# Kernel optimization log

Hardware: AMD Instinct MI355X
Metric: run time of the kernel (lower is better)

Reference implementation:

```python
import jax, jax.numpy as jnp
import numpy as np

N, E, G, H, R, L = 10000, 320000, 16, 128, 32, 3
NUM_TYPES = 60
CUTOFF = 5.0


def setup_inputs() -> dict:
    key = jax.random.key(0)
    ks = jax.random.split(key, 32)
    s = 1.0 / np.sqrt(H)

    def w(k, shape, scale):
        return jax.random.normal(k, shape, jnp.float32) * scale

    return {
        'z': jax.random.randint(ks[0], (N,), 0, NUM_TYPES),
        'pos': jax.random.normal(ks[1], (N, 3), jnp.float32) * 3.0,
        'edge_index': jax.random.randint(ks[2], (2, E), 0, N),
        'batch': jnp.sort(jax.random.randint(ks[3], (N,), 0, G)),
        # learned params (per-layer params stacked on leading L axis)
        'emb': w(ks[4], (NUM_TYPES, H), 0.1),
        'atomic_ref': jnp.zeros((NUM_TYPES, 1), jnp.float32),
        'W_msg': w(ks[5], (L, H, H), s), 'b_msg': jnp.zeros((L, H), jnp.float32),
        'W_rbf': w(ks[6], (L, R, H), 1.0 / np.sqrt(R)),
        'Wg1': w(ks[7], (L, 2 * H + R, H), 1.0 / np.sqrt(2 * H + R)),
        'bg1': jnp.zeros((L, H), jnp.float32),
        'Wgv': w(ks[8], (L, H, H), s),
        'Wg2': w(ks[9], (L, H, H), s), 'bg2': jnp.zeros((L, H), jnp.float32),
        'Wd1': w(ks[10], (L, H, H), s), 'bd1': jnp.zeros((L, H), jnp.float32),
        'Wd2': w(ks[11], (L, H, H), s), 'bd2': jnp.zeros((L, H), jnp.float32),
        'Wr1': w(ks[12], (L, H, H), s), 'br1': jnp.zeros((L, H), jnp.float32),
        'Wr2': w(ks[13], (L, H, 1), s), 'br2': jnp.zeros((L, 1), jnp.float32),
        'num_graphs': G,
    }


def _rbf(d):
    # Gaussian radial basis with cosine cutoff envelope.  d: [E]
    centers = jnp.linspace(0.0, CUTOFF, R, dtype=d.dtype)
    gamma = (R / CUTOFF) ** 2
    fcut = 0.5 * (jnp.cos(jnp.pi * d / CUTOFF) + 1.0) * (d < CUTOFF)
    return jnp.exp(-gamma * (d[:, None] - centers) ** 2) * fcut[:, None]  # [E,R]


def reference(z, pos, edge_index, batch, emb, atomic_ref, W_msg, b_msg, W_rbf,
              Wg1, bg1, Wgv, Wg2, bg2, Wd1, bd1, Wd2, bd2, Wr1, br1, Wr2, br2,
              num_graphs):
    row, col = edge_index[0], edge_index[1]
    vec = pos[col] - pos[row]                       # [E,3] edge vectors
    d = jnp.clip(jnp.linalg.norm(vec, axis=-1), 1e-8, None)
    r_hat = vec / d[:, None]                        # [E,3]
    rbf = _rbf(d)                                   # [E,R]

    h0 = emb[z]                                     # [N,H] scalar features
    h1 = jnp.zeros((z.shape[0], 3, H), h0.dtype)    # [N,3,H] l=1 features
    e_tot = jnp.zeros((num_graphs, 1), h0.dtype)

    n_nodes = z.shape[0]
    for l in range(L):
        # LeibnizCoupling: radial-filtered edge messages
        m = (h0[col] @ W_msg[l] + b_msg[l]) * (rbf @ W_rbf[l])      # [E,H]
        # PhysicsGating: gate from endpoint scalars, rbf, and projected l=1 feats
        s1 = jnp.einsum('ech,ec->eh', h1[row], r_hat)               # [E,H]
        g_in = jnp.concatenate([h0[row], h0[col], rbf], axis=-1)
        pre = jax.nn.silu(g_in @ Wg1[l] + bg1[l] + s1 @ Wgv[l])
        gate = jax.nn.sigmoid(pre @ Wg2[l] + bg2[l])                # [E,H]
        gm = gate * m
        # CartesianDensityBlock: scatter messages to nodes
        agg = jax.ops.segment_sum(gm, row, num_segments=n_nodes)    # [N,H]
        delta_h0 = jax.nn.silu(agg @ Wd1[l] + bd1[l]) @ Wd2[l] + bd2[l]
        delta_h1 = jax.ops.segment_sum(r_hat[:, :, None] * gm[:, None, :],
                                       row, num_segments=n_nodes)   # [N,3,H]
        h0 = h0 + delta_h0
        h1 = h1 + delta_h1
        # per-layer readout -> per-graph energy
        e_atom = jax.nn.silu(h0 @ Wr1[l] + br1[l]) @ Wr2[l] + br2[l]  # [N,1]
        e_tot = e_tot + jax.ops.segment_sum(e_atom, batch, num_segments=num_graphs)

    e_tot = e_tot + jax.ops.segment_sum(atomic_ref[z], batch, num_segments=num_graphs)
    return e_tot
```

## Files before the change

kernel.cpp:

```cpp
#include <hip/hip_runtime.h>

#define HDIM 128
#define RDIM 32
#define BE   64
#define SB   2048

typedef __attribute__((ext_vector_type(8))) short s8v;
typedef __attribute__((ext_vector_type(4))) float f4v;

__device__ __forceinline__ float sigm(float x){ return 1.0f/(1.0f+__expf(-x)); }
__device__ __forceinline__ float silu_f(float x){ return x*sigm(x); }
__device__ __forceinline__ float4 f4z(){ return make_float4(0.f,0.f,0.f,0.f); }

__device__ __forceinline__ unsigned short f2bf(float x){
  unsigned u = __float_as_uint(x);
  unsigned r = u + 0x7FFFu + ((u>>16)&1u);
  return (unsigned short)(r>>16);
}
__device__ __forceinline__ float bf2f(unsigned short b){
  return __uint_as_float(((unsigned)b)<<16);
}

#define FMA4C(D, sc, W) do{ (D).x=fmaf((sc),(W).x,(D).x); (D).y=fmaf((sc),(W).y,(D).y); \
                            (D).z=fmaf((sc),(W).z,(D).z); (D).w=fmaf((sc),(W).w,(D).w);}while(0)
#define LERP4ADD(D, A0, A1, f) do{ \
  (D).x += fmaf((f),(A1).x-(A0).x,(A0).x); (D).y += fmaf((f),(A1).y-(A0).y,(A0).y); \
  (D).z += fmaf((f),(A1).z-(A0).z,(A0).z); (D).w += fmaf((f),(A1).w-(A0).w,(A0).w);}while(0)

__global__ __launch_bounds__(256) void k_init(const int* __restrict__ z,
                                              const float* __restrict__ emb,
                                              const int* __restrict__ batch,
                                              const float* __restrict__ aref,
                                              float* __restrict__ eout,
                                              float* __restrict__ h0,
                                              float* __restrict__ h1, int N, int G){
  __shared__ float bins[256];
  const int b = blockIdx.x, t = threadIdx.x;
  const int idx = b*256 + t;
  if (idx < N*HDIM){ int n = idx>>7, h = idx&127; h0[idx] = emb[z[n]*HDIM + h]; }
  if (idx < N*384) h1[idx] = 0.f;
  if (b < (N+255)/256){
    for (int i=t;i<G;i+=256) bins[i]=0.f;
    __syncthreads();
    if (idx < N) atomicAdd(&bins[batch[idx]], aref[z[idx]]);
    __syncthreads();
    for (int i=t;i<G;i+=256) if (bins[i]!=0.f) unsafeAtomicAdd(&eout[i], bins[i]);
  }
}

__global__ __launch_bounds__(256) void k_geom(const float* __restrict__ pos,
                                              const int* __restrict__ eidx, int E,
                                              int* __restrict__ ecnt,
                                              int* __restrict__ erow, int* __restrict__ ecol,
                                              float* __restrict__ erx, float* __restrict__ ery,
                                              float* __restrict__ erz, float* __restrict__ ed,
                                              int* __restrict__ cnt){
  __shared__ int scan[256];
  __shared__ int sbase;
  int t = threadIdx.x;
  int e = blockIdx.x*256 + t;
  int alive = 0; float dx=0,dy=0,dz=0,d=1.f; int row=0,col=0;
  if (e < E){
    row = eidx[e]; col = eidx[E+e];
    float ax=pos[row*3+0], ay=pos[row*3+1], az=pos[row*3+2];
    float bx=pos[col*3+0], by=pos[col*3+1], bz=pos[col*3+2];
    dx=bx-ax; dy=by-ay; dz=bz-az;
    d = sqrtf(dx*dx+dy*dy+dz*dz);
    d = fmaxf(d, 1e-8f);
    alive = (d < 5.0f) ? 1 : 0;
  }
  scan[t]=alive; __syncthreads();
  for (int off=1; off<256; off<<=1){
    int v = (t>=off)? scan[t-off] : 0;
    __syncthreads();
    if (t>=off) scan[t]+=v;
    __syncthreads();
  }
  if (t==255) sbase = atomicAdd(ecnt, scan[255]);
  __syncthreads();
  if (alive){
    int p = sbase + scan[t]-1;
    erow[p]=row; ecol[p]=col;
    float inv = 1.0f/d;
    erx[p]=dx*inv; ery[p]=dy*inv; erz[p]=dz*inv;
    ed[p]=d;
    atomicAdd(&cnt[row], 1);
  }
}

__global__ __launch_bounds__(1024) void k_scan(const int* __restrict__ cnt,
                                               int* __restrict__ estart, int N){
  __shared__ int ps[1024];
  const int t = threadIdx.x;
  const int CH = (N + 1023)/1024;
  const int base = t*CH;
  int s = 0;
  for (int i=0;i<CH;i++){ int idx=base+i; if(idx<N) s += cnt[idx]; }
  ps[t] = s; __syncthreads();
  for (int off=1; off<1024; off<<=1){
    int v = (t>=off)? ps[t-off]:0;
    __syncthreads();
    ps[t]+=v;
    __syncthreads();
  }
  int run = (t==0)? 0 : ps[t-1];
  for (int i=0;i<CH;i++){
    int idx=base+i;
    if (idx<N){ estart[idx]=run; run += cnt[idx]; }
  }
  if (t==1023) estart[N] = ps[1023];
}

__global__ __launch_bounds__(256) void k_fill(const int* __restrict__ ecnt,
                                              const int* __restrict__ erow,
                                              const int* __restrict__ ecol,
                                              const float* __restrict__ erx,
                                              const float* __restrict__ ery,
                                              const float* __restrict__ erz,
                                              const float* __restrict__ ed,
                                              const int* __restrict__ estart,
                                              int* __restrict__ fillc, int CAP,
                                              int* __restrict__ srow, int* __restrict__ scol,
                                              float* __restrict__ srx, float* __restrict__ sry,
                                              float* __restrict__ srz, float* __restrict__ sd){
  int e = blockIdx.x*256 + threadIdx.x;
  if (e < ecnt[0]){
    int r = erow[e];
    int pos = estart[r] + atomicAdd(&fillc[r], 1);
    if (pos < CAP){
      srow[pos]=r; scol[pos]=ecol[e];
      srx[pos]=erx[e]; sry[pos]=ery[e]; srz[pos]=erz[e]; sd[pos]=ed[e];
    }
  }
}

__global__ __launch_bounds__(128) void k_lutcvt(const float* __restrict__ Wg1,
                                                const float* __restrict__ Wrbf,
                                                float* __restrict__ Tg, float* __restrict__ Tr,
                                                const float* __restrict__ Wmsg,
                                                const float* __restrict__ Wgv,
                                                const float* __restrict__ Wd1,
                                                const float* __restrict__ Wd2,
                                                const float* __restrict__ Wr1,
                                                const float* __restrict__ Wg2,
                                                unsigned short* __restrict__ WT, int L){
  const int b = blockIdx.x;
  if (b < L*SB){
    const int l = b / SB;
    const int s = b % SB;
    __shared__ float rbf[RDIM];
    const float d = s * (5.0f/(SB-1));
    if (threadIdx.x < RDIM){
      float fc = 0.5f*(__cosf(0.62831853071f*d)+1.0f);
      float td = d - 0.16129032258f*threadIdx.x;
      rbf[threadIdx.x] = __expf(-40.96f*td*td)*fc;
    }
    __syncthreads();
    const int c = threadIdx.x;
    const float* Wg = Wg1 + (size_t)l*288*HDIM + 256*HDIM;
    const float* Wr = Wrbf + (size_t)l*RDIM*HDIM;
    float sg=0.f, sr=0.f;
    #pragma unroll
    for (int r=0;r<RDIM;r++){
      sg = fmaf(rbf[r], Wg[r*HDIM+c], sg);
      sr = fmaf(rbf[r], Wr[r*HDIM+c], sr);
    }
    Tg[((size_t)l*SB+s)*HDIM + c] = sg;
    Tr[((size_t)l*SB+s)*HDIM + c] = sr;
    return;
  }
  const int base = (b - L*SB)*1024;
  #pragma unroll
  for (int u=0;u<8;u++){
    int idx = base + u*128 + threadIdx.x;
    if (idx >= L*8*16384) return;
    int l = idx / (8*16384);
    int rem = idx % (8*16384);
    int mat = rem >> 14;
    int nk = rem & 16383;
    int n = nk >> 7, k = nk & 127;
    float v;
    switch(mat){
      case 0: v = Wmsg[(size_t)l*16384 + k*128 + n]; break;
      case 1: v = Wg1 [(size_t)l*288*128 + k*128 + n]; break;
      case 2: v = Wg1 [(size_t)l*288*128 + (128+k)*128 + n]; break;
      case 3: v = Wgv [(size_t)l*16384 + k*128 + n]; break;
      case 4: v = Wd1 [(size_t)l*16384 + k*128 + n]; break;
      case 5: v = Wd2 [(size_t)l*16384 + k*128 + n]; break;
      case 6: v = Wr1 [(size_t)l*16384 + k*128 + n]; break;
      default: v = Wg2[(size_t)l*16384 + k*128 + n]; break;
    }
    WT[idx] = f2bf(v);
  }
}

__device__ __forceinline__ void stage32p(float (*WS)[132], const float* __restrict__ W, int t){
  int r = t>>3, c0 = (t&7)*16;
  const float4* src = (const float4*)&W[(size_t)r*HDIM + c0];
  float4* dst = (float4*)&WS[r][c0];
  #pragma unroll
  for (int u=0;u<4;u++) dst[u]=src[u];
}

__device__ __forceinline__ void load_tile(float (*S)[132], const float* __restrict__ src,
                                          int nb, int N, int stride, int t){
  #pragma unroll
  for (int u=0;u<4;u++){
    int p = t + 256*u;
    int r = p>>5, c4 = p&31;
    float4 v = f4z();
    if (nb + r < N) v = *(const float4*)&src[(size_t)(nb+r)*stride + c4*4];
    *(float4*)&S[r][c4*4] = v;
  }
}

__device__ __forceinline__ void load_tile16(unsigned short (*S)[136], const float* __restrict__ src,
                                            int nb, int N, int stride, int t){
  #pragma unroll
  for (int u=0;u<4;u++){
    int p = t + 256*u;
    int r = p>>5, c4 = p&31;
    float4 v = f4z();
    if (nb + r < N) v = *(const float4*)&src[(size_t)(nb+r)*stride + c4*4];
    ushort4 pk; pk.x=f2bf(v.x); pk.y=f2bf(v.y); pk.z=f2bf(v.z); pk.w=f2bf(v.w);
    *(ushort4*)&S[r][c4*4] = pk;
  }
}

__device__ __forceinline__ void gemm_lds(const float (*AS)[132], float (*WS)[132],
                                         const float* __restrict__ W, const float* __restrict__ bias,
                                         int r, int cg, int t, float4 (&acc)[4]){
  float4 b = bias ? *(const float4*)&bias[4*cg] : f4z();
  #pragma unroll
  for (int i=0;i<4;i++) acc[i] = b;
  for (int kt=0; kt<4; kt++){
    stage32p(WS, W + (size_t)kt*32*HDIM, t);
    __syncthreads();
    #pragma unroll
    for (int k4=0;k4<8;k4++){
      float4 w0 = *(const float4*)&WS[4*k4+0][4*cg];
      float4 w1 = *(const float4*)&WS[4*k4+1][4*cg];
      float4 w2 = *(const float4*)&WS[4*k4+2][4*cg];
      float4 w3 = *(const float4*)&WS[4*k4+3][4*cg];
      #pragma unroll
      for (int i=0;i<4;i++){
        float4 a4 = *(const float4*)&AS[r+8*i][kt*32+4*k4];
        FMA4C(acc[i], a4.x, w0); FMA4C(acc[i], a4.y, w1);
        FMA4C(acc[i], a4.z, w2); FMA4C(acc[i], a4.w, w3);
      }
    }
    __syncthreads();
  }
}

__device__ __forceinline__ void mfma32(const unsigned short (*A16)[136],
                                       unsigned short (*WTs)[40],
                                       const unsigned short* __restrict__ WT,
                                       int t, f4v (&acc)[2][2]){
  const int lane = t&63, w = t>>6;
  const int l15 = lane&15, lk = lane>>4;
  for (int kt=0; kt<4; kt++){
    int n = t>>1, ch = t&1;
    *(s8v*)&WTs[n][ch*16]     = *(const s8v*)&WT[(size_t)n*HDIM + kt*32 + ch*16];
    *(s8v*)&WTs[n][ch*16 + 8] = *(const s8v*)&WT[(size_t)n*HDIM + kt*32 + ch*16 + 8];
    __syncthreads();
    s8v a0 = *(const s8v*)&A16[l15][kt*32 + lk*8];
    s8v a1 = *(const s8v*)&A16[16+l15][kt*32 + lk*8];
    s8v b0 = *(const s8v*)&WTs[w*32 +  0 + l15][lk*8];
    s8v b1 = *(const s8v*)&WTs[w*32 + 16 + l15][lk*8];
    acc[0][0] = __builtin_amdgcn_mfma_f32_16x16x32_bf16(a0, b0, acc[0][0], 0, 0, 0);
    acc[0][1] = __builtin_amdgcn_mfma_f32_16x16x32_bf16(a0, b1, acc[0][1], 0, 0, 0);
    acc[1][0] = __builtin_amdgcn_mfma_f32_16x16x32_bf16(a1, b0, acc[1][0], 0, 0, 0);
    acc[1][1] = __builtin_amdgcn_mfma_f32_16x16x32_bf16(a1, b1, acc[1][1], 0, 0, 0);
    __syncthreads();
  }
}

__device__ __forceinline__ void mfma16(const unsigned short (*A16)[136],
                                       unsigned short (*WTs)[40],
                                       const unsigned short* __restrict__ WT,
                                       int t, f4v (&acc)[2]){
  const int lane = t&63, w = t>>6;
  const int l15 = lane&15, lk = lane>>4;
  for (int kt=0; kt<4; kt++){
    int n = t>>1, ch = t&1;
    *(s8v*)&WTs[n][ch*16]     = *(const s8v*)&WT[(size_t)n*HDIM + kt*32 + ch*16];
    *(s8v*)&WTs[n][ch*16 + 8] = *(const s8v*)&WT[(size_t)n*HDIM + kt*32 + ch*16 + 8];
    __syncthreads();
    s8v a0 = *(const s8v*)&A16[l15][kt*32 + lk*8];
    s8v b0 = *(const s8v*)&WTs[w*32 +  0 + l15][lk*8];
    s8v b1 = *(const s8v*)&WTs[w*32 + 16 + l15][lk*8];
    acc[0] = __builtin_amdgcn_mfma_f32_16x16x32_bf16(a0, b0, acc[0], 0, 0, 0);
    acc[1] = __builtin_amdgcn_mfma_f32_16x16x32_bf16(a0, b1, acc[1], 0, 0, 0);
    __syncthreads();
  }
}

__global__ __launch_bounds__(256) void k_node_pre(const float* __restrict__ h0,
                                                  const float* __restrict__ h1,
                                                  const unsigned short* __restrict__ WTl,
                                                  const float* __restrict__ bmsg,
                                                  const float* __restrict__ bg1,
                                                  const float* __restrict__ Wr1p, const float* __restrict__ br1p,
                                                  const float* __restrict__ Wr2p, const float* __restrict__ br2p,
                                                  const int* __restrict__ batch, float* __restrict__ eout,
                                                  int G, int doRead,
                                                  float* __restrict__ hm, float* __restrict__ ga,
                                                  float* __restrict__ gb, float* __restrict__ hv, int N){
  __shared__ char smem[34816];
  const int t = threadIdx.x;
  const int g = blockIdx.y;
  const int nb = blockIdx.x*32;

  if (g == 6){
    if (!doRead) return;
    float (*AS)[132] = (float(*)[132])smem;
    float (*WS)[132] = (float(*)[132])(smem + 16896);
    float* ebins     = (float*)(smem + 33792);
    const int r = t>>5, cg = t&31;
    float4 acc[4];
    for (int i=t;i<G;i+=256) ebins[i]=0.f;
    load_tile(AS, h0, nb, N, HDIM, t);
    __syncthreads();
    gemm_lds(AS, WS, Wr1p, br1p, r, cg, t, acc);
    const float4 w2 = *(const float4*)&Wr2p[4*cg];
    float part[4];
    #pragma unroll
    for (int i=0;i<4;i++){
      float4 u;
      u.x=silu_f(acc[i].x); u.y=silu_f(acc[i].y);
      u.z=silu_f(acc[i].z); u.w=silu_f(acc[i].w);
      part[i] = u.x*w2.x + u.y*w2.y + u.z*w2.z + u.w*w2.w;
    }
    #pragma unroll
    for (int off=16; off>=1; off>>=1){
      #pragma unroll
      for (int i=0;i<4;i++) part[i] += __shfl_down(part[i], off, 32);
    }
    if (cg == 0){
      #pragma unroll
      for (int i=0;i<4;i++){
        int n = nb + r + 8*i;
        if (n < N) atomicAdd(&ebins[batch[n]], part[i] + br2p[0]);
      }
    }
    __syncthreads();
    for (int i=t;i<G;i+=256) if (ebins[i]!=0.f) unsafeAtomicAdd(&eout[i], ebins[i]);
    return;
  }

  unsigned short (*AS16)[136] = (unsigned short(*)[136])smem;
  unsigned short (*WTs)[40]   = (unsigned short(*)[40])(smem + 8704);

  const float* A; int astride;
  const float* bias;
  float* out; int ostride; int ooff; int mat;
  if (g < 3){
    A = h0; astride = HDIM;
    if (g==0){ mat = 0; bias = bmsg; out = hm; }
    else if (g==1){ mat = 1; bias = bg1;  out = ga; }
    else { mat = 2; bias = nullptr; out = gb; }
    ostride = HDIM; ooff = 0;
  } else {
    int c = g-3;
    A = h1 + c*HDIM; astride = 384;
    mat = 3; bias = nullptr;
    out = hv; ostride = 384; ooff = c*HDIM;
  }

  load_tile16(AS16, A, nb, N, astride, t);
  __syncthreads();

  f4v zz = {0.f,0.f,0.f,0.f};
  f4v acc[2][2]; acc[0][0]=zz; acc[0][1]=zz; acc[1][0]=zz; acc[1][1]=zz;
  mfma32(AS16, WTs, WTl + (size_t)mat*16384, t, acc);

  const int lane = t&63, w = t>>6, l15 = lane&15, lk = lane>>4;
  #pragma unroll
  for (int m=0;m<2;m++){
    #pragma unroll
    for (int ct=0;ct<2;ct++){
      int c = w*32 + ct*16 + l15;
      float bv = bias ? bias[c] : 0.f;
      #pragma unroll
      for (int reg=0;reg<4;reg++){
        int n = nb + m*16 + lk*4 + reg;
        if (n < N) out[(size_t)n*ostride + ooff + c] = acc[m][ct][reg] + bv;
      }
    }
  }
}

__global__ __launch_bounds__(256) void k_readout(const float* __restrict__ h0,
                                                 const float* __restrict__ Wr1, const float* __restrict__ br1,
                                                 const float* __restrict__ Wr2, const float* __restrict__ br2,
                                                 const int* __restrict__ batch, float* __restrict__ eout,
                                                 int N, int G){
  __shared__ float AS[32][132];
  __shared__ float WS[32][132];
  __shared__ float ebins[256];
  const int t = threadIdx.x;
  const int nb = blockIdx.x*32;
  const int r = t>>5, cg = t&31;
  float4 acc[4];
  for (int i=t;i<G;i+=256) ebins[i]=0.f;
  load_tile(AS, h0, nb, N, HDIM, t);
  __syncthreads();
  gemm_lds(AS, WS, Wr1, br1, r, cg, t, acc);
  const float4 w2 = *(const float4*)&Wr2[4*cg];
  float part[4];
  #pragma unroll
  for (int i=0;i<4;i++){
    float4 u;
    u.x=silu_f(acc[i].x); u.y=silu_f(acc[i].y);
    u.z=silu_f(acc[i].z); u.w=silu_f(acc[i].w);
    part[i] = u.x*w2.x + u.y*w2.y + u.z*w2.z + u.w*w2.w;
  }
  #pragma unroll
  for (int off=16; off>=1; off>>=1){
    #pragma unroll
    for (int i=0;i<4;i++) part[i] += __shfl_down(part[i], off, 32);
  }
  if (cg == 0){
    #pragma unroll
    for (int i=0;i<4;i++){
      int n = nb + r + 8*i;
      if (n < N) atomicAdd(&ebins[batch[n]], part[i] + br2[0]);
    }
  }
  __syncthreads();
  for (int i=t;i<G;i+=256) if (ebins[i]!=0.f) unsafeAtomicAdd(&eout[i], ebins[i]);
}

__global__ __launch_bounds__(512) void k_edge_gm(const int* __restrict__ ecnt, int CAP,
                                                 const int* __restrict__ srow, const int* __restrict__ scol,
                                                 const float* __restrict__ srx, const float* __restrict__ sry,
                                                 const float* __restrict__ srz, const float* __restrict__ sd,
                                                 const float* __restrict__ hm, const float* __restrict__ ga,
                                                 const float* __restrict__ gb, const float* __restrict__ hv,
                                                 const float* __restrict__ Tg,  const float* __restrict__ Tr,
                                                 const unsigned short* __restrict__ Wg2T,
                                                 const float* __restrict__ bg2,
                                                 unsigned short* __restrict__ gm_s){
  __shared__ unsigned short preA[BE][136];
  __shared__ unsigned short WTs[128][40];
  __shared__ int   rowS[BE], colS[BE];
  __shared__ float rhS[3][BE];
  __shared__ float fS[BE];
  __shared__ int   iS[BE];

  const int t = threadIdx.x;
  int ec = ecnt[0]; if (ec > CAP) ec = CAP;
  const int base = blockIdx.x*BE;
  if (base >= ec) return;

  if (t < BE){
    int eg = base + t;
    bool ok = eg < ec;
    rowS[t] = ok ? srow[eg] : 0;
    colS[t] = ok ? scol[eg] : 0;
    rhS[0][t] = ok ? srx[eg] : 0.f;
    rhS[1][t] = ok ? sry[eg] : 0.f;
    rhS[2][t] = ok ? srz[eg] : 0.f;
    float d = ok ? sd[eg] : 0.f;
    float u = d * ((float)(SB-1)/5.0f);
    int i = (int)u; if (i > SB-2) i = SB-2;
    iS[t] = i; fS[t] = u - (float)i;
  }
  __syncthreads();

  {
    const int e = t>>3, q = t&7;
    const int eg = base + e;
    const bool ok = eg < ec;
    const int row = rowS[e], col = colS[e];
    const float rx = rhS[0][e], ry = rhS[1][e], rz = rhS[2][e];
    const float ff = fS[e];
    const float4* tg0 = (const float4*)(Tg + (size_t)iS[e]*HDIM);
    const float4* tg1 = tg0 + (HDIM/4);
    const float4* gaR = (const float4*)(ga + (size_t)row*HDIM);
    const float4* gbR = (const float4*)(gb + (size_t)col*HDIM);
    const float4* hv0 = (const float4*)(hv + (size_t)row*384);
    const float4* hv1 = hv0 + 32;
    const float4* hv2 = hv0 + 64;
    #pragma unroll
    for (int j=0;j<4;j++){
      int cb = q + 8*j;
      float4 v = f4z();
      if (ok){
        float4 A = gaR[cb], B = gbR[cb];
        float4 V0 = hv0[cb], V1 = hv1[cb], V2 = hv2[cb];
        v.x = A.x+B.x; v.y = A.y+B.y; v.z = A.z+B.z; v.w = A.w+B.w;
        FMA4C(v, rx, V0); FMA4C(v, ry, V1); FMA4C(v, rz, V2);
        float4 a0 = tg0[cb], a1 = tg1[cb];
        LERP4ADD(v, a0, a1, ff);
        v.x = silu_f(v.x); v.y = silu_f(v.y); v.z = silu_f(v.z); v.w = silu_f(v.w);
      }
      ushort4 pk;
      pk.x = f2bf(v.x); pk.y = f2bf(v.y); pk.z = f2bf(v.z); pk.w = f2bf(v.w);
      *(ushort4*)&preA[e][4*cb] = pk;
    }
  }
  __syncthreads();

  const int lane = t & 63;
  const int w    = t >> 6;
  const int wm   = w & 3;
  const int wn   = w >> 2;
  const int l15  = lane & 15;
  const int lk   = lane >> 4;
  f4v acc0 = {0.f,0.f,0.f,0.f}, acc1 = acc0, acc2 = acc0, acc3 = acc0;

  for (int kt=0; kt<4; kt++){
    {
      int n = t>>2, ch = t&3;
      *(s8v*)&WTs[n][ch*8] = *(const s8v*)&Wg2T[(size_t)n*HDIM + kt*32 + ch*8];
    }
    __syncthreads();
    s8v a = *(const s8v*)&preA[wm*16 + l15][kt*32 + lk*8];
    s8v b0 = *(const s8v*)&WTs[wn*64 +  0 + l15][lk*8];
    s8v b1 = *(const s8v*)&WTs[wn*64 + 16 + l15][lk*8];
    s8v b2 = *(const s8v*)&WTs[wn*64 + 32 + l15][lk*8];
    s8v b3 = *(const s8v*)&WTs[wn*64 + 48 + l15][lk*8];
    acc0 = __builtin_amdgcn_mfma_f32_16x16x32_bf16(a, b0, acc0, 0, 0, 0);
    acc1 = __builtin_amdgcn_mfma_f32_16x16x32_bf16(a, b1, acc1, 0, 0, 0);
    acc2 = __builtin_amdgcn_mfma_f32_16x16x32_bf16(a, b2, acc2, 0, 0, 0);
    acc3 = __builtin_amdgcn_mfma_f32_16x16x32_bf16(a, b3, acc3, 0, 0, 0);
    __syncthreads();
  }

  {
    #pragma unroll
    for (int reg=0; reg<4; reg++){
      int m = lk*4 + reg;
      int e = wm*16 + m;
      preA[e][wn*64 +  0 + l15] = f2bf(acc0[reg]);
      preA[e][wn*64 + 16 + l15] = f2bf(acc1[reg]);
      preA[e][wn*64 + 32 + l15] = f2bf(acc2[reg]);
      preA[e][wn*64 + 48 + l15] = f2bf(acc3[reg]);
    }
  }
  __syncthreads();

  const int cg = t&31;
  const int e0 = (t>>5)*4;
  const float4 bg = *(const float4*)&bg2[4*cg];
  #pragma unroll
  for (int i=0;i<4;i++){
    int e = e0 + i;
    int eg = base + e;
    if (eg >= ec) continue;
    int col = colS[e];
    const float ff = fS[e];
    const float4* tr0 = (const float4*)(Tr + (size_t)iS[e]*HDIM);
    const float4* tr1 = tr0 + (HDIM/4);
    float4 r0 = tr0[cg], r1 = tr1[cg];
    float4 rw;
    rw.x = fmaf(ff, r1.x-r0.x, r0.x); rw.y = fmaf(ff, r1.y-r0.y, r0.y);
    rw.z = fmaf(ff, r1.z-r0.z, r0.z); rw.w = fmaf(ff, r1.w-r0.w, r0.w);
    float4 hmv = *(const float4*)&hm[(size_t)col*HDIM + 4*cg];
    ushort4 gp4 = *(const ushort4*)&preA[e][4*cg];
    float4 g;
    g.x = sigm(bf2f(gp4.x) + bg.x); g.y = sigm(bf2f(gp4.y) + bg.y);
    g.z = sigm(bf2f(gp4.z) + bg.z); g.w = sigm(bf2f(gp4.w) + bg.w);
    ushort4 pk;
    pk.x = f2bf(g.x*hmv.x*rw.x); pk.y = f2bf(g.y*hmv.y*rw.y);
    pk.z = f2bf(g.z*hmv.z*rw.z); pk.w = f2bf(g.w*hmv.w*rw.w);
    *(ushort4*)&gm_s[(size_t)eg*HDIM + 4*cg] = pk;
  }
}

__global__ __launch_bounds__(256) void k_node_post(float* __restrict__ h0, float* __restrict__ h1,
                                                   const int* __restrict__ estart, int CAP,
                                                   const unsigned short* __restrict__ gm_s,
                                                   const float* __restrict__ srx,
                                                   const float* __restrict__ sry,
                                                   const float* __restrict__ srz,
                                                   const unsigned short* __restrict__ WTd1,
                                                   const float* __restrict__ bd1,
                                                   const unsigned short* __restrict__ WTd2,
                                                   const float* __restrict__ bd2,
                                                   int N){
  __shared__ char smem[23040];
  float (*aS)[132]            = (float(*)[132])smem;
  unsigned short (*AS16)[136] = (unsigned short(*)[136])(smem+8448);
  unsigned short (*WTs)[40]   = (unsigned short(*)[40])(smem+12800);
  unsigned short (*tS16)[136] = (unsigned short(*)[136])smem;
  const int t = threadIdx.x;
  const int nb = blockIdx.x*16;

  {
    const int nl = t>>4, s = t&15;
    const int n = nb + nl;
    float4 ag[2], v0[2], v1[2], v2[2];
    #pragma unroll
    for (int j=0;j<2;j++){ ag[j]=f4z(); v0[j]=f4z(); v1[j]=f4z(); v2[j]=f4z(); }
    if (n < N){
      int p0 = estart[n];
      int p1 = estart[n+1]; if (p1 > CAP) p1 = CAP;
      for (int p=p0; p<p1; ++p){
        float rx = srx[p], ry = sry[p], rz = srz[p];
        const ushort4* gp = (const ushort4*)&gm_s[(size_t)p*HDIM + 8*s];
        #pragma unroll
        for (int j=0;j<2;j++){
          ushort4 pk = gp[j];
          float4 g;
          g.x = bf2f(pk.x); g.y = bf2f(pk.y); g.z = bf2f(pk.z); g.w = bf2f(pk.w);
          ag[j].x+=g.x; ag[j].y+=g.y; ag[j].z+=g.z; ag[j].w+=g.w;
          FMA4C(v0[j], rx, g); FMA4C(v1[j], ry, g); FMA4C(v2[j], rz, g);
        }
      }
    }
    #pragma unroll
    for (int j=0;j<2;j++) *(float4*)&aS[nl][8*s+4*j] = ag[j];
    if (n < N){
      #pragma unroll
      for (int j=0;j<2;j++){
        size_t b = (size_t)n*384 + 8*s + 4*j;
        float4 a0 = *(const float4*)&h1[b];
        float4 a1 = *(const float4*)&h1[b+128];
        float4 a2 = *(const float4*)&h1[b+256];
        a0.x+=v0[j].x; a0.y+=v0[j].y; a0.z+=v0[j].z; a0.w+=v0[j].w;
        a1.x+=v1[j].x; a1.y+=v1[j].y; a1.z+=v1[j].z; a1.w+=v1[j].w;
        a2.x+=v2[j].x; a2.y+=v2[j].y; a2.z+=v2[j].z; a2.w+=v2[j].w;
        *(float4*)&h1[b]     = a0;
        *(float4*)&h1[b+128] = a1;
        *(float4*)&h1[b+256] = a2;
      }
    }
  }
  __syncthreads();

  {
    #pragma unroll
    for (int u=0;u<2;u++){
      int p = t + 256*u;
      int r = p>>5, c4 = p&31;
      float4 v = *(const float4*)&aS[r][c4*4];
      ushort4 pk; pk.x=f2bf(v.x); pk.y=f2bf(v.y); pk.z=f2bf(v.z); pk.w=f2bf(v.w);
      *(ushort4*)&AS16[r][c4*4] = pk;
    }
  }
  __syncthreads();

  const int lane = t&63, w = t>>6, l15 = lane&15, lk = lane>>4;
  f4v zz = {0.f,0.f,0.f,0.f};
  f4v acc[2]; acc[0]=zz; acc[1]=zz;

  mfma16((const unsigned short(*)[136])AS16, WTs, WTd1, t, acc);
  #pragma unroll
  for (int ct=0;ct<2;ct++){
    int c = w*32 + ct*16 + l15;
    float bv = bd1[c];
    #pragma unroll
    for (int reg=0;reg<4;reg++){
      int rr = lk*4 + reg;
      tS16[rr][c] = f2bf(silu_f(acc[ct][reg] + bv));
    }
  }
  __syncthreads();

  acc[0]=zz; acc[1]=zz;
  mfma16((const unsigned short(*)[136])tS16, WTs, WTd2, t, acc);
  #pragma unroll
  for (int ct=0;ct<2;ct++){
    int c = w*32 + ct*16 + l15;
    float bv = bd2[c];
    #pragma unroll
    for (int reg=0;reg<4;reg++){
      int n = nb + lk*4 + reg;
      if (n < N) h0[(size_t)n*HDIM + c] += acc[ct][reg] + bv;
    }
  }
}

extern "C" void kernel_launch(void* const* d_in, const int* in_sizes, int n_in,
                              void* d_out, int out_size, void* d_ws, size_t ws_size,
                              hipStream_t stream){
  const int*   z     = (const int*)  d_in[0];
  const float* pos   = (const float*)d_in[1];
  const int*   eidx  = (const int*)  d_in[2];
  const int*   batch = (const int*)  d_in[3];
  const float* emb   = (const float*)d_in[4];
  const float* aref  = (const float*)d_in[5];
  const float* Wmsg  = (const float*)d_in[6];
  const float* bmsg  = (const float*)d_in[7];
  const float* Wrbf  = (const float*)d_in[8];
  const float* Wg1   = (const float*)d_in[9];
  const float* bg1   = (const float*)d_in[10];
  const float* Wgv   = (const float*)d_in[11];
  const float* Wg2   = (const float*)d_in[12];
  const float* bg2   = (const float*)d_in[13];
  const float* Wd1   = (const float*)d_in[14];
  const float* bd1   = (const float*)d_in[15];
  const float* Wd2   = (const float*)d_in[16];
  const float* bd2   = (const float*)d_in[17];
  const float* Wr1   = (const float*)d_in[18];
  const float* br1   = (const float*)d_in[19];
  const float* Wr2   = (const float*)d_in[20];
  const float* br2   = (const float*)d_in[21];
  const int N = in_sizes[0];
  const int E = in_sizes[2]/2;
  const int G = out_size;
  const int L = 3;
  const int CAP = (int)(((long long)E*7)/16);
  float* out = (float*)d_out;

  char* ws = (char*)d_ws;
  size_t off = 0;
  auto carve = [&](size_t bytes)->char*{
    char* p = ws + off; off += (bytes + 255) & ~(size_t)255; return p;
  };
  char*  zero0  = ws;
  int*   ecnt   = (int*)  carve(sizeof(int));
  int*   cnt    = (int*)  carve((size_t)N*4);
  int*   fillc  = (int*)  carve((size_t)N*4);
  size_t zlen   = off;
  int*   erow   = (int*)  carve((size_t)E*4);
  int*   ecol   = (int*)  carve((size_t)E*4);
  float* erx    = (float*)carve((size_t)E*4);
  float* ery    = (float*)carve((size_t)E*4);
  float* erz    = (float*)carve((size_t)E*4);
  float* ed     = (float*)carve((size_t)E*4);
  int*   estart = (int*)  carve((size_t)(N+1)*4);
  int*   srow   = (int*)  carve((size_t)CAP*4);
  int*   scol   = (int*)  carve((size_t)CAP*4);
  float* srx    = (float*)carve((size_t)CAP*4);
  float* sry    = (float*)carve((size_t)CAP*4);
  float* srz    = (float*)carve((size_t)CAP*4);
  float* sd     = (float*)carve((size_t)CAP*4);
  unsigned short* gm_s = (unsigned short*)carve((size_t)CAP*HDIM*2);
  unsigned short* WT   = (unsigned short*)carve((size_t)L*8*HDIM*HDIM*2);
  float* Tg     = (float*)carve((size_t)L*SB*HDIM*4);
  float* Tr     = (float*)carve((size_t)L*SB*HDIM*4);
  float* h0     = (float*)carve((size_t)N*HDIM*4);
  float* h1b    = (float*)carve((size_t)N*384*4);
  float* hm     = (float*)carve((size_t)N*HDIM*4);
  float* ga     = (float*)carve((size_t)N*HDIM*4);
  float* gb     = (float*)carve((size_t)N*HDIM*4);
  float* hvb    = (float*)carve((size_t)N*384*4);

  (void)hipMemsetAsync(zero0, 0, zlen, stream);
  (void)hipMemsetAsync(out,   0, (size_t)G*4, stream);

  k_init<<<(N*384+255)/256, 256, 0, stream>>>(z, emb, batch, aref, out, h0, h1b, N, G);
  k_geom<<<(E+255)/256, 256, 0, stream>>>(pos, eidx, E, ecnt, erow, ecol, erx, ery, erz, ed, cnt);
  {
    int cvt_blocks = (L*8*16384 + 1023)/1024;
    k_lutcvt<<<L*SB + cvt_blocks, 128, 0, stream>>>(Wg1, Wrbf, Tg, Tr,
                                                    Wmsg, Wgv, Wd1, Wd2, Wr1, Wg2, WT, L);
  }
  k_scan<<<1, 1024, 0, stream>>>(cnt, estart, N);
  k_fill<<<(E+255)/256, 256, 0, stream>>>(ecnt, erow, ecol, erx, ery, erz, ed,
                                          estart, fillc, CAP,
                                          srow, scol, srx, sry, srz, sd);

  const int nblk   = (N+31)/32;
  const int nblk16 = (N+15)/16;
  const int eblk   = (CAP + BE-1)/BE;
  for (int l=0; l<L; ++l){
    const int lp = (l>0) ? (l-1) : 0;
    const unsigned short* WTl = WT + (size_t)l*8*16384;
    k_node_pre<<<dim3(nblk,7), 256, 0, stream>>>(h0, h1b,
        WTl,
        bmsg + (size_t)l*HDIM, bg1 + (size_t)l*HDIM,
        Wr1 + (size_t)lp*HDIM*HDIM, br1 + (size_t)lp*HDIM,
        Wr2 + (size_t)lp*HDIM, br2 + lp,
        batch, out, G, (l>0) ? 1 : 0,
        hm, ga, gb, hvb, N);
    k_edge_gm<<<eblk, 512, 0, stream>>>(ecnt, CAP, srow, scol, srx, sry, srz, sd,
        hm, ga, gb, hvb,
        Tg + (size_t)l*SB*HDIM, Tr + (size_t)l*SB*HDIM,
        WTl + (size_t)7*16384, bg2 + (size_t)l*HDIM,
        gm_s);
    k_node_post<<<nblk16, 256, 0, stream>>>(h0, h1b, estart, CAP, gm_s, srx, sry, srz,
        WTl + (size_t)4*16384, bd1 + (size_t)l*HDIM,
        WTl + (size_t)5*16384, bd2 + (size_t)l*HDIM,
        N);
  }
  k_readout<<<nblk, 256, 0, stream>>>(h0,
      Wr1 + (size_t)(L-1)*HDIM*HDIM, br1 + (size_t)(L-1)*HDIM,
      Wr2 + (size_t)(L-1)*HDIM, br2 + (L-1),
      batch, out, N, G);
}
```

Before: 328.4 us.

## Fuse node-post, next-layer node-pre projections and readout into one kernel

Merges the per-layer node update (aggregation plus Wd1/Wd2 MLP), the next layer's node projections (Wmsg, Wg1 halves, Wgv on h1) and the energy readout into a single kernel working on 16-node tiles. The updated h0 and h1 stay in LDS as bf16, so they are not re-read from global memory, and two launches per layer are removed. The readout GEMM moves from an fp32 FMA path to bf16 MFMA, which costs some precision. Each fused block now runs many sequential small GEMMs, which may lower parallelism compared with the separate 2D-grid node_pre launch.

```diff
diff --git a/kernel.cpp b/kernel.cpp
--- a/kernel.cpp
+++ b/kernel.cpp
@@ -194,26 +194,6 @@
   }
 }
 
-__device__ __forceinline__ void stage32p(float (*WS)[132], const float* __restrict__ W, int t){
-  int r = t>>3, c0 = (t&7)*16;
-  const float4* src = (const float4*)&W[(size_t)r*HDIM + c0];
-  float4* dst = (float4*)&WS[r][c0];
-  #pragma unroll
-  for (int u=0;u<4;u++) dst[u]=src[u];
-}
-
-__device__ __forceinline__ void load_tile(float (*S)[132], const float* __restrict__ src,
-                                          int nb, int N, int stride, int t){
-  #pragma unroll
-  for (int u=0;u<4;u++){
-    int p = t + 256*u;
-    int r = p>>5, c4 = p&31;
-    float4 v = f4z();
-    if (nb + r < N) v = *(const float4*)&src[(size_t)(nb+r)*stride + c4*4];
-    *(float4*)&S[r][c4*4] = v;
-  }
-}
-
 __device__ __forceinline__ void load_tile16(unsigned short (*S)[136], const float* __restrict__ src,
                                             int nb, int N, int stride, int t){
   #pragma unroll
@@ -227,32 +207,6 @@
   }
 }
 
-__device__ __forceinline__ void gemm_lds(const float (*AS)[132], float (*WS)[132],
-                                         const float* __restrict__ W, const float* __restrict__ bias,
-                                         int r, int cg, int t, float4 (&acc)[4]){
-  float4 b = bias ? *(const float4*)&bias[4*cg] : f4z();
-  #pragma unroll
-  for (int i=0;i<4;i++) acc[i] = b;
-  for (int kt=0; kt<4; kt++){
-    stage32p(WS, W + (size_t)kt*32*HDIM, t);
-    __syncthreads();
-    #pragma unroll
-    for (int k4=0;k4<8;k4++){
-      float4 w0 = *(const float4*)&WS[4*k4+0][4*cg];
-      float4 w1 = *(const float4*)&WS[4*k4+1][4*cg];
-      float4 w2 = *(const float4*)&WS[4*k4+2][4*cg];
-      float4 w3 = *(const float4*)&WS[4*k4+3][4*cg];
-      #pragma unroll
-      for (int i=0;i<4;i++){
-        float4 a4 = *(const float4*)&AS[r+8*i][kt*32+4*k4];
-        FMA4C(acc[i], a4.x, w0); FMA4C(acc[i], a4.y, w1);
-        FMA4C(acc[i], a4.z, w2); FMA4C(acc[i], a4.w, w3);
-      }
-    }
-    __syncthreads();
-  }
-}
-
 __device__ __forceinline__ void mfma32(const unsigned short (*A16)[136],
                                        unsigned short (*WTs)[40],
                                        const unsigned short* __restrict__ WT,
@@ -301,56 +255,13 @@
                                                   const unsigned short* __restrict__ WTl,
                                                   const float* __restrict__ bmsg,
                                                   const float* __restrict__ bg1,
-                                                  const float* __restrict__ Wr1p, const float* __restrict__ br1p,
-                                                  const float* __restrict__ Wr2p, const float* __restrict__ br2p,
-                                                  const int* __restrict__ batch, float* __restrict__ eout,
-                                                  int G, int doRead,
                                                   float* __restrict__ hm, float* __restrict__ ga,
                                                   float* __restrict__ gb, float* __restrict__ hv, int N){
-  __shared__ char smem[34816];
+  __shared__ unsigned short AS16[32][136];
+  __shared__ unsigned short WTs[128][40];
   const int t = threadIdx.x;
   const int g = blockIdx.y;
   const int nb = blockIdx.x*32;
-
-  if (g == 6){
-    if (!doRead) return;
-    float (*AS)[132] = (float(*)[132])smem;
-    float (*WS)[132] = (float(*)[132])(smem + 16896);
-    float* ebins     = (float*)(smem + 33792);
-    const int r = t>>5, cg = t&31;
-    float4 acc[4];
-    for (int i=t;i<G;i+=256) ebins[i]=0.f;
-    load_tile(AS, h0, nb, N, HDIM, t);
-    __syncthreads();
-    gemm_lds(AS, WS, Wr1p, br1p, r, cg, t, acc);
-    const float4 w2 = *(const float4*)&Wr2p[4*cg];
-    float part[4];
-    #pragma unroll
-    for (int i=0;i<4;i++){
-      float4 u;
-      u.x=silu_f(acc[i].x); u.y=silu_f(acc[i].y);
-      u.z=silu_f(acc[i].z); u.w=silu_f(acc[i].w);
-      part[i] = u.x*w2.x + u.y*w2.y + u.z*w2.z + u.w*w2.w;
-    }
-    #pragma unroll
-    for (int off=16; off>=1; off>>=1){
-      #pragma unroll
-      for (int i=0;i<4;i++) part[i] += __shfl_down(part[i], off, 32);
-    }
-    if (cg == 0){
-      #pragma unroll
-      for (int i=0;i<4;i++){
-        int n = nb + r + 8*i;
-        if (n < N) atomicAdd(&ebins[batch[n]], part[i] + br2p[0]);
-      }
-    }
-    __syncthreads();
-    for (int i=t;i<G;i+=256) if (ebins[i]!=0.f) unsafeAtomicAdd(&eout[i], ebins[i]);
-    return;
-  }
-
-  unsigned short (*AS16)[136] = (unsigned short(*)[136])smem;
-  unsigned short (*WTs)[40]   = (unsigned short(*)[40])(smem + 8704);
 
   const float* A; int astride;
   const float* bias;
@@ -373,7 +284,7 @@
 
   f4v zz = {0.f,0.f,0.f,0.f};
   f4v acc[2][2]; acc[0][0]=zz; acc[0][1]=zz; acc[1][0]=zz; acc[1][1]=zz;
-  mfma32(AS16, WTs, WTl + (size_t)mat*16384, t, acc);
+  mfma32((const unsigned short(*)[136])AS16, WTs, WTl + (size_t)mat*16384, t, acc);
 
   const int lane = t&63, w = t>>6, l15 = lane&15, lk = lane>>4;
   #pragma unroll
@@ -389,47 +300,6 @@
       }
     }
   }
-}
-
-__global__ __launch_bounds__(256) void k_readout(const float* __restrict__ h0,
-                                                 const float* __restrict__ Wr1, const float* __restrict__ br1,
-                                                 const float* __restrict__ Wr2, const float* __restrict__ br2,
-                                                 const int* __restrict__ batch, float* __restrict__ eout,
-                                                 int N, int G){
-  __shared__ float AS[32][132];
-  __shared__ float WS[32][132];
-  __shared__ float ebins[256];
-  const int t = threadIdx.x;
-  const int nb = blockIdx.x*32;
-  const int r = t>>5, cg = t&31;
-  float4 acc[4];
-  for (int i=t;i<G;i+=256) ebins[i]=0.f;
-  load_tile(AS, h0, nb, N, HDIM, t);
-  __syncthreads();
-  gemm_lds(AS, WS, Wr1, br1, r, cg, t, acc);
-  const float4 w2 = *(const float4*)&Wr2[4*cg];
-  float part[4];
-  #pragma unroll
-  for (int i=0;i<4;i++){
-    float4 u;
-    u.x=silu_f(acc[i].x); u.y=silu_f(acc[i].y);
-    u.z=silu_f(acc[i].z); u.w=silu_f(acc[i].w);
-    part[i] = u.x*w2.x + u.y*w2.y + u.z*w2.z + u.w*w2.w;
-  }
-  #pragma unroll
-  for (int off=16; off>=1; off>>=1){
-    #pragma unroll
-    for (int i=0;i<4;i++) part[i] += __shfl_down(part[i], off, 32);
-  }
-  if (cg == 0){
-    #pragma unroll
-    for (int i=0;i<4;i++){
-      int n = nb + r + 8*i;
-      if (n < N) atomicAdd(&ebins[batch[n]], part[i] + br2[0]);
-    }
-  }
-  __syncthreads();
-  for (int i=t;i<G;i+=256) if (ebins[i]!=0.f) unsafeAtomicAdd(&eout[i], ebins[i]);
 }
 
 __global__ __launch_bounds__(512) void k_edge_gm(const int* __restrict__ ecnt, int CAP,
@@ -570,24 +440,36 @@
   }
 }
 
-__global__ __launch_bounds__(256) void k_node_post(float* __restrict__ h0, float* __restrict__ h1,
-                                                   const int* __restrict__ estart, int CAP,
-                                                   const unsigned short* __restrict__ gm_s,
-                                                   const float* __restrict__ srx,
-                                                   const float* __restrict__ sry,
-                                                   const float* __restrict__ srz,
-                                                   const unsigned short* __restrict__ WTd1,
-                                                   const float* __restrict__ bd1,
-                                                   const unsigned short* __restrict__ WTd2,
-                                                   const float* __restrict__ bd2,
-                                                   int N){
-  __shared__ char smem[23040];
-  float (*aS)[132]            = (float(*)[132])smem;
-  unsigned short (*AS16)[136] = (unsigned short(*)[136])(smem+8448);
-  unsigned short (*WTs)[40]   = (unsigned short(*)[40])(smem+12800);
-  unsigned short (*tS16)[136] = (unsigned short(*)[136])smem;
+__global__ __launch_bounds__(256) void k_fused(float* __restrict__ h0, float* __restrict__ h1,
+                                               const int* __restrict__ estart, int CAP,
+                                               const unsigned short* __restrict__ gm_s,
+                                               const float* __restrict__ srx,
+                                               const float* __restrict__ sry,
+                                               const float* __restrict__ srz,
+                                               const unsigned short* __restrict__ WTcur,
+                                               const unsigned short* __restrict__ WTnxt,
+                                               const float* __restrict__ bd1,
+                                               const float* __restrict__ bd2,
+                                               const float* __restrict__ bmsgN,
+                                               const float* __restrict__ bg1N,
+                                               const float* __restrict__ br1,
+                                               const float* __restrict__ Wr2,
+                                               const float* __restrict__ br2p,
+                                               const int* __restrict__ batch,
+                                               float* __restrict__ eout, int G,
+                                               float* __restrict__ hm, float* __restrict__ ga,
+                                               float* __restrict__ gb, float* __restrict__ hv,
+                                               int doPre, int N){
+  __shared__ unsigned short AS16[16][136];
+  __shared__ unsigned short h0S[16][136];
+  __shared__ unsigned short h1S[3][16][136];
+  __shared__ unsigned short WTs[128][40];
+  __shared__ float ebins[256];
   const int t = threadIdx.x;
   const int nb = blockIdx.x*16;
+  const int lane = t&63, w = t>>6, l15 = lane&15, lk = lane>>4;
+
+  for (int i=t;i<256;i+=256) ebins[i]=0.f;
 
   {
     const int nl = t>>4, s = t&15;
@@ -612,7 +494,11 @@
       }
     }
     #pragma unroll
-    for (int j=0;j<2;j++) *(float4*)&aS[nl][8*s+4*j] = ag[j];
+    for (int j=0;j<2;j++){
+      ushort4 pk;
+      pk.x=f2bf(ag[j].x); pk.y=f2bf(ag[j].y); pk.z=f2bf(ag[j].z); pk.w=f2bf(ag[j].w);
+      *(ushort4*)&AS16[nl][8*s+4*j] = pk;
+    }
     if (n < N){
       #pragma unroll
       for (int j=0;j<2;j++){
@@ -626,42 +512,42 @@
         *(float4*)&h1[b]     = a0;
         *(float4*)&h1[b+128] = a1;
         *(float4*)&h1[b+256] = a2;
+        ushort4 p0s; p0s.x=f2bf(a0.x); p0s.y=f2bf(a0.y); p0s.z=f2bf(a0.z); p0s.w=f2bf(a0.w);
+        ushort4 p1s; p1s.x=f2bf(a1.x); p1s.y=f2bf(a1.y); p1s.z=f2bf(a1.z); p1s.w=f2bf(a1.w);
+        ushort4 p2s; p2s.x=f2bf(a2.x); p2s.y=f2bf(a2.y); p2s.z=f2bf(a2.z); p2s.w=f2bf(a2.w);
+        *(ushort4*)&h1S[0][nl][8*s+4*j] = p0s;
+        *(ushort4*)&h1S[1][nl][8*s+4*j] = p1s;
+        *(ushort4*)&h1S[2][nl][8*s+4*j] = p2s;
       }
-    }
-  }
-  __syncthreads();
-
-  {
-    #pragma unroll
-    for (int u=0;u<2;u++){
-      int p = t + 256*u;
-      int r = p>>5, c4 = p&31;
-      float4 v = *(const float4*)&aS[r][c4*4];
-      ushort4 pk; pk.x=f2bf(v.x); pk.y=f2bf(v.y); pk.z=f2bf(v.z); pk.w=f2bf(v.w);
-      *(ushort4*)&AS16[r][c4*4] = pk;
-    }
-  }
-  __syncthreads();
-
-  const int lane = t&63, w = t>>6, l15 = lane&15, lk = lane>>4;
+    } else {
+      ushort4 zq = {0,0,0,0};
+      #pragma unroll
+      for (int j=0;j<2;j++){
+        *(ushort4*)&h1S[0][nl][8*s+4*j] = zq;
+        *(ushort4*)&h1S[1][nl][8*s+4*j] = zq;
+        *(ushort4*)&h1S[2][nl][8*s+4*j] = zq;
+      }
+    }
+  }
+  __syncthreads();
+
   f4v zz = {0.f,0.f,0.f,0.f};
-  f4v acc[2]; acc[0]=zz; acc[1]=zz;
-
-  mfma16((const unsigned short(*)[136])AS16, WTs, WTd1, t, acc);
+  f4v acc[2];
+
+  acc[0]=zz; acc[1]=zz;
+  mfma16((const unsigned short(*)[136])AS16, WTs, WTcur + (size_t)4*16384, t, acc);
   #pragma unroll
   for (int ct=0;ct<2;ct++){
     int c = w*32 + ct*16 + l15;
     float bv = bd1[c];
     #pragma unroll
-    for (int reg=0;reg<4;reg++){
-      int rr = lk*4 + reg;
-      tS16[rr][c] = f2bf(silu_f(acc[ct][reg] + bv));
-    }
+    for (int reg=0;reg<4;reg++)
+      h0S[lk*4+reg][c] = f2bf(silu_f(acc[ct][reg] + bv));
   }
   __syncthreads();
 
   acc[0]=zz; acc[1]=zz;
-  mfma16((const unsigned short(*)[136])tS16, WTs, WTd2, t, acc);
+  mfma16((const unsigned short(*)[136])h0S, WTs, WTcur + (size_t)5*16384, t, acc);
   #pragma unroll
   for (int ct=0;ct<2;ct++){
     int c = w*32 + ct*16 + l15;
@@ -669,9 +555,76 @@
     #pragma unroll
     for (int reg=0;reg<4;reg++){
       int n = nb + lk*4 + reg;
-      if (n < N) h0[(size_t)n*HDIM + c] += acc[ct][reg] + bv;
-    }
-  }
+      float h = (n<N) ? h0[(size_t)n*HDIM + c] : 0.f;
+      h += acc[ct][reg] + bv;
+      if (n<N) h0[(size_t)n*HDIM + c] = h;
+      h0S[lk*4+reg][c] = f2bf(h);
+    }
+  }
+  __syncthreads();
+
+  if (doPre){
+    #pragma unroll
+    for (int mat=0; mat<3; mat++){
+      const float* bias = (mat==0)? bmsgN : (mat==1)? bg1N : nullptr;
+      float* out = (mat==0)? hm : (mat==1)? ga : gb;
+      acc[0]=zz; acc[1]=zz;
+      mfma16((const unsigned short(*)[136])h0S, WTs, WTnxt + (size_t)mat*16384, t, acc);
+      #pragma unroll
+      for (int ct=0;ct<2;ct++){
+        int c = w*32 + ct*16 + l15;
+        float bv = bias ? bias[c] : 0.f;
+        #pragma unroll
+        for (int reg=0;reg<4;reg++){
+          int n = nb + lk*4 + reg;
+          if (n<N) out[(size_t)n*HDIM + c] = acc[ct][reg] + bv;
+        }
+      }
+      __syncthreads();
+    }
+    #pragma unroll
+    for (int cdim=0; cdim<3; cdim++){
+      acc[0]=zz; acc[1]=zz;
+      mfma16((const unsigned short(*)[136])h1S[cdim], WTs, WTnxt + (size_t)3*16384, t, acc);
+      #pragma unroll
+      for (int ct=0;ct<2;ct++){
+        int c = w*32 + ct*16 + l15;
+        #pragma unroll
+        for (int reg=0;reg<4;reg++){
+          int n = nb + lk*4 + reg;
+          if (n<N) hv[(size_t)n*384 + cdim*HDIM + c] = acc[ct][reg];
+        }
+      }
+      __syncthreads();
+    }
+  }
+
+  acc[0]=zz; acc[1]=zz;
+  mfma16((const unsigned short(*)[136])h0S, WTs, WTcur + (size_t)6*16384, t, acc);
+  #pragma unroll
+  for (int ct=0;ct<2;ct++){
+    int c = w*32 + ct*16 + l15;
+    float bv = br1[c];
+    #pragma unroll
+    for (int reg=0;reg<4;reg++)
+      AS16[lk*4+reg][c] = f2bf(silu_f(acc[ct][reg] + bv));
+  }
+  __syncthreads();
+  {
+    const int nl = t>>4, s = t&15;
+    const int n = nb + nl;
+    float part = 0.f;
+    #pragma unroll
+    for (int i=0;i<8;i++){
+      int c = 8*s + i;
+      part = fmaf(bf2f(AS16[nl][c]), Wr2[c], part);
+    }
+    #pragma unroll
+    for (int off=8; off>=1; off>>=1) part += __shfl_down(part, off, 16);
+    if (s==0 && n<N) atomicAdd(&ebins[batch[n]], part + br2p[0]);
+  }
+  __syncthreads();
+  for (int i=t;i<G;i+=256) if (ebins[i]!=0.f) unsafeAtomicAdd(&eout[i], ebins[i]);
 }
 
 extern "C" void kernel_launch(void* const* d_in, const int* in_sizes, int n_in,
@@ -758,28 +711,26 @@
   const int nblk   = (N+31)/32;
   const int nblk16 = (N+15)/16;
   const int eblk   = (CAP + BE-1)/BE;
+
+  k_node_pre<<<dim3(nblk,6), 256, 0, stream>>>(h0, h1b,
+      WT, bmsg, bg1, hm, ga, gb, hvb, N);
+
   for (int l=0; l<L; ++l){
-    const int lp = (l>0) ? (l-1) : 0;
-    const unsigned short* WTl = WT + (size_t)l*8*16384;
-    k_node_pre<<<dim3(nblk,7), 256, 0, stream>>>(h0, h1b,
-        WTl,
-        bmsg + (size_t)l*HDIM, bg1 + (size_t)l*HDIM,
-        Wr1 + (size_t)lp*HDIM*HDIM, br1 + (size_t)lp*HDIM,
-        Wr2 + (size_t)lp*HDIM, br2 + lp,
-        batch, out, G, (l>0) ? 1 : 0,
-        hm, ga, gb, hvb, N);
+    const unsigned short* WTcur = WT + (size_t)l*8*16384;
+    const int ln = (l<L-1) ? (l+1) : l;
+    const unsigned short* WTnxt = WT + (size_t)ln*8*16384;
     k_edge_gm<<<eblk, 512, 0, stream>>>(ecnt, CAP, srow, scol, srx, sry, srz, sd,
         hm, ga, gb, hvb,
         Tg + (size_t)l*SB*HDIM, Tr + (size_t)l*SB*HDIM,
-        WTl + (size_t)7*16384, bg2 + (size_t)l*HDIM,
+        WTcur + (size_t)7*16384, bg2 + (size_t)l*HDIM,
         gm_s);
-    k_node_post<<<nblk16, 256, 0, stream>>>(h0, h1b, estart, CAP, gm_s, srx, sry, srz,
-        WTl + (size_t)4*16384, bd1 + (size_t)l*HDIM,
-        WTl + (size_t)5*16384, bd2 + (size_t)l*HDIM,
-        N);
-  }
-  k_readout<<<nblk, 256, 0, stream>>>(h0,
-      Wr1 + (size_t)(L-1)*HDIM*HDIM, br1 + (size_t)(L-1)*HDIM,
-      Wr2 + (size_t)(L-1)*HDIM, br2 + (L-1),
-      batch, out, N, G);
-}
+    k_fused<<<nblk16, 256, 0, stream>>>(h0, h1b, estart, CAP, gm_s, srx, sry, srz,
+        WTcur, WTnxt,
+        bd1 + (size_t)l*HDIM, bd2 + (size_t)l*HDIM,
+        bmsg + (size_t)ln*HDIM, bg1 + (size_t)ln*HDIM,
+        br1 + (size_t)l*HDIM, Wr2 + (size_t)l*HDIM, br2 + l,
+        batch, out, G,
+        hm, ga, gb, hvb,
+        (l<L-1) ? 1 : 0, N);
+  }
+}
```

After: 283.3 us, median of 2. -13.7%, faster.
